# Kernel optimization log

Hardware: AMD Instinct MI355X
Metric: run time of the kernel (lower is better)

Reference implementation:

```python
import jax, jax.numpy as jnp
import numpy as np

B, ROWS, COLS, D, H = 64, 7, 7, 1280, 256
S, NEG, GRU_ROWS = 5, 16, 6  # pred_steps, neg_samples, rows processed by GRU


def setup_inputs() -> dict:
    key = jax.random.key(0)
    ks = jax.random.split(key, 10)
    sc = 0.05  # keep gates/tanh out of saturation
    return {
        "encodings": jax.random.normal(ks[0], (B, ROWS, COLS, D), jnp.float32),
        "hidden": jnp.zeros((1, 1, H), jnp.float32),
        "gru_w_ih": jax.random.normal(ks[1], (3 * H, D), jnp.float32) * sc,
        "gru_w_hh": jax.random.normal(ks[2], (3 * H, H), jnp.float32) * sc,
        "gru_b_ih": jax.random.normal(ks[3], (3 * H,), jnp.float32) * sc,
        "gru_b_hh": jax.random.normal(ks[4], (3 * H,), jnp.float32) * sc,
        "wk_w": jax.random.normal(ks[5], (S, D, H), jnp.float32) * sc,
        "wk_b": jax.random.normal(ks[6], (S, D), jnp.float32) * sc,
        "neg_rows": jax.random.randint(ks[7], (B, S, GRU_ROWS, COLS, NEG), 0, ROWS, jnp.int32),
        "neg_cols": jax.random.randint(ks[8], (B, S, GRU_ROWS, COLS, NEG), 0, COLS, jnp.int32),
    }


def _gru_contexts(encodings, hidden, w_ih, w_hh, b_ih, b_hh):
    # One GRU run per (image, column) over the first 6 rows, all batched together.
    x_seq = jnp.transpose(encodings[:, :GRU_ROWS], (1, 0, 2, 3)).reshape(GRU_ROWS, B * COLS, D)
    h0 = jnp.broadcast_to(hidden.reshape(1, H), (B * COLS, H))

    def step(h, x):
        gi = x @ w_ih.T + b_ih          # [N, 3H]
        gh = h @ w_hh.T + b_hh
        i_r, i_z, i_n = jnp.split(gi, 3, axis=-1)
        h_r, h_z, h_n = jnp.split(gh, 3, axis=-1)
        r = jax.nn.sigmoid(i_r + h_r)
        z = jax.nn.sigmoid(i_z + h_z)
        n = jnp.tanh(i_n + r * h_n)
        h_new = (1.0 - z) * n + z * h
        return h_new, h_new

    _, cs = jax.lax.scan(step, h0, x_seq)              # [6, B*7, H]
    return jnp.transpose(cs.reshape(GRU_ROWS, B, COLS, H), (1, 0, 2, 3))  # [B,6,7,H]


def reference(encodings, hidden, gru_w_ih, gru_w_hh, gru_b_ih, gru_b_hh,
              wk_w, wk_b, neg_rows, neg_cols):
    contexts = _gru_contexts(encodings, hidden, gru_w_ih, gru_w_hh, gru_b_ih, gru_b_hh)

    # Predictions for every step/row/col: hardtanh(Wk[s] c + b)   [B,S,6,7,D]
    preds = jnp.clip(jnp.einsum("brch,sdh->bsrcd", contexts, wk_w)
                     + wk_b[None, :, None, None, :], -1.0, 1.0)

    # Dot of every prediction with every patch encoding of the same image.
    enc_flat = encodings.reshape(B, ROWS * COLS, D)
    dots_all = jnp.einsum("bsrcd,bqd->bsrcq", preds, enc_flat)  # [B,S,6,7,49]

    # Positive: target is encodings[img, row, col] (as in the source).
    qpos = (jnp.arange(GRU_ROWS)[:, None] * COLS + jnp.arange(COLS)[None, :])  # [6,7]
    pos = jnp.take_along_axis(dots_all, qpos[None, None, :, :, None], axis=-1)  # [B,S,6,7,1]

    # Negatives: random (row,col) patches of the same image.
    neg_q = neg_rows * COLS + neg_cols                            # [B,S,6,7,NEG]
    neg = jnp.take_along_axis(dots_all, neg_q, axis=-1)

    dots = jnp.concatenate([pos, neg], axis=-1)                   # [B,S,6,7,1+NEG]
    loss_each = -jax.nn.log_softmax(dots, axis=-1)[..., 0]
    correct = (jnp.argmax(dots, axis=-1) == 0).astype(jnp.float32)

    # Valid predictions: row in range(6 - step)
    mask = ((jnp.arange(S)[:, None] + jnp.arange(GRU_ROWS)[None, :]) < GRU_ROWS)
    mask = mask.astype(jnp.float32)[None, :, :, None]             # [1,S,6,1]
    num_preds = jnp.sum(mask) * B * COLS

    loss = jnp.sum(loss_each * mask) / num_preds
    acc = jnp.sum(correct * mask) / num_preds
    return loss, acc
```

## Files before the change

kernel.cpp:

```cpp
#include <hip/hip_runtime.h>
#include <math.h>


typedef __bf16 bf16x8 __attribute__((ext_vector_type(8)));
typedef float  f32x4  __attribute__((ext_vector_type(4)));
typedef unsigned short u16;
typedef unsigned int u32;

__device__ inline u16 f2bf(float f) {
  unsigned int u = __float_as_uint(f);
  u += 0x7fff + ((u >> 16) & 1);
  return (u16)(u >> 16);
}

__device__ inline float bf2f(u16 b) {
  u32 u = (u32)b << 16;
  return __builtin_bit_cast(float, u);
}

__device__ inline void f2bf8(const float* s, u16* o) {
  float4 v0 = *(const float4*)s, v1 = *(const float4*)(s + 4);
  o[0] = f2bf(v0.x); o[1] = f2bf(v0.y); o[2] = f2bf(v0.z); o[3] = f2bf(v0.w);
  o[4] = f2bf(v1.x); o[5] = f2bf(v1.y); o[6] = f2bf(v1.z); o[7] = f2bf(v1.w);
}

__device__ inline bf16x8 lds_frag(const char* sm, int off) {
  return __builtin_bit_cast(bf16x8, *(const uint4*)(sm + off));
}

__device__ inline void gld_lds16(const void* g, void* l) {
  __builtin_amdgcn_global_load_lds(
      (const __attribute__((address_space(1))) u32*)g,
      (__attribute__((address_space(3))) u32*)l, 16, 0, 0);
}

__device__ inline float fast_sigmoid(float x) {
  float t = __builtin_amdgcn_exp2f(-1.44269504f * x);
  return __builtin_amdgcn_rcpf(1.f + t);
}
__device__ inline float fast_tanh(float x) {
  float xc = fminf(fmaxf(x, -9.f), 9.f);
  float t = __builtin_amdgcn_exp2f(2.88539008f * xc);
  return (t - 1.f) * __builtin_amdgcn_rcpf(t + 1.f);
}
__device__ inline float fast_exp(float x) {
  return __builtin_amdgcn_exp2f(1.44269504f * x);
}
__device__ inline float fast_log(float x) {
  return __builtin_amdgcn_logf(x) * 0.69314718f;
}

#define MFMA16(a, b, c) __builtin_amdgcn_mfma_f32_16x16x32_bf16(a, b, c, 0, 0, 0)

__global__ __launch_bounds__(256) void pack_all(
    const float* __restrict__ w_hh, const float* __restrict__ wk_w,
    const float* __restrict__ enc,  const float* __restrict__ w_ih,
    u16* __restrict__ whhpk, u16* __restrict__ wkwpk, u16* __restrict__ epk,
    u16* __restrict__ enc2,  u16* __restrict__ wih2, float* __restrict__ out)
{
  int tid = blockIdx.x * 256 + threadIdx.x;
  int lane = tid & 63;
  if (tid == 0) { out[0] = 0.f; out[1] = 0.f; }
  u16 o[8];
  if (tid < 24576) {
    int rest = tid >> 6;
    int cb = rest >> 3, ks = rest & 7;
    int w = cb / 6, nf = cb % 6;
    int g = nf >> 1, half = nf & 1;
    int col = g * 256 + w * 32 + half * 16 + (lane & 15);
    int k = ks * 32 + (lane >> 4) * 8;
    f2bf8(&w_hh[(size_t)col * 256 + k], o);
    *(uint4*)&whhpk[(size_t)tid * 8] = *(uint4*)o;
  } else if (tid < 229376) {
    int u = tid - 24576;
    int f = u >> 6;
    int ks = f & 7, t1 = f >> 3;
    int w = t1 & 3, t2 = t1 >> 2;
    int ch = t2 % 20, s = t2 / 20;
    f2bf8(&wk_w[((size_t)s * 1280 + ch * 64 + w * 16 + (lane & 15)) * 256
                + ks * 32 + (lane >> 4) * 8], o);
    *(uint4*)&wkwpk[(size_t)f * 512 + lane * 8] = *(uint4*)o;
  } else if (tid < 884736) {
    int u = tid - 229376;
    int f = u >> 6;
    int ks2 = f & 1, t1 = f >> 1;
    int w = t1 & 3, t2 = t1 >> 2;
    int ch = t2 % 20, b = t2 / 20;
    int q = w * 16 + (lane & 15);
    if (q < 49) {
      f2bf8(&enc[(size_t)(b * 49 + q) * 1280 + ch * 64 + ks2 * 32 + (lane >> 4) * 8], o);
    } else {
#pragma unroll
      for (int j = 0; j < 8; ++j) o[j] = 0;
    }
    *(uint4*)&epk[(size_t)f * 512 + lane * 8] = *(uint4*)o;
  } else if (tid < 1314816) {
    int u = tid - 884736;
    int unit = u & 1023;
    int row = unit >> 3, sl = unit & 7;
    int tk = u >> 10;
    int k0 = tk % 20, by = tk / 20;
    int m = by * 128 + row;
    int r = m / 448, n = m - r * 448;
    int b = n / 7, c = n - b * 7;
    int slot = sl ^ (row & 7);
    f2bf8(&enc[(size_t)(b * 49 + r * 7 + c) * 1280 + k0 * 64 + slot * 8], o);
    *(uint4*)&enc2[(size_t)u * 8] = *(uint4*)o;
  } else if (tid < 1437696) {
    int u = tid - 1314816;
    int unit = u & 1023;
    int row = unit >> 3, sl = unit & 7;
    int tk = u >> 10;
    int k0 = tk % 20, bx = tk / 20;
    int slot = sl ^ (row & 7);
    f2bf8(&w_ih[(size_t)(bx * 128 + row) * 1280 + k0 * 64 + slot * 8], o);
    *(uint4*)&wih2[(size_t)u * 8] = *(uint4*)o;
  }
}

__global__ __launch_bounds__(256) void gi_mfma(
    const u16* __restrict__ enc2, const u16* __restrict__ wih2,
    const float* __restrict__ b_ih, u16* __restrict__ gib)
{
  const int bx = blockIdx.x, by = blockIdx.y;
  const int t = threadIdx.x, lane = t & 63, w = t >> 6;
  const int wr = w >> 1, wc = w & 1;

  __shared__ char sm[32768];
  const int A_OFF = 0, B_OFF = 16384;
  const int wu = t & ~63;

  f32x4 acc[4][4];
#pragma unroll
  for (int i = 0; i < 4; ++i)
#pragma unroll
    for (int j = 0; j < 4; ++j) acc[i][j] = (f32x4){0.f, 0.f, 0.f, 0.f};

  for (int k0c = 0; k0c < 20; ++k0c) {
    if (k0c) __syncthreads();
    const char* ga = (const char*)enc2 + ((size_t)(by * 20 + k0c) << 14);
    const char* gb = (const char*)wih2 + ((size_t)(bx * 20 + k0c) << 14);
#pragma unroll
    for (int j = 0; j < 4; ++j) {
      gld_lds16(ga + (j * 256 + t) * 16, sm + A_OFF + (j * 256 + wu) * 16);
      gld_lds16(gb + (j * 256 + t) * 16, sm + B_OFF + (j * 256 + wu) * 16);
    }
    __syncthreads();
#pragma unroll
    for (int ks = 0; ks < 2; ++ks) {
      bf16x8 a[4], b[4];
#pragma unroll
      for (int i = 0; i < 4; ++i) {
        int arow = wr * 64 + i * 16 + (lane & 15);
        int akb  = (ks * 64 + (lane >> 4) * 16) ^ ((arow & 7) << 4);
        a[i] = lds_frag(sm, A_OFF + arow * 128 + akb);
        int brow = wc * 64 + i * 16 + (lane & 15);
        int bkb  = (ks * 64 + (lane >> 4) * 16) ^ ((brow & 7) << 4);
        b[i] = lds_frag(sm, B_OFF + brow * 128 + bkb);
      }
#pragma unroll
      for (int i = 0; i < 4; ++i)
#pragma unroll
        for (int jn = 0; jn < 4; ++jn)
          acc[i][jn] = MFMA16(a[i], b[jn], acc[i][jn]);
    }
  }

#pragma unroll
  for (int i = 0; i < 4; ++i)
#pragma unroll
    for (int jn = 0; jn < 4; ++jn) {
      int gcol = bx * 128 + wc * 64 + jn * 16 + (lane & 15);
      float bias = b_ih[gcol];
#pragma unroll
      for (int r4 = 0; r4 < 4; ++r4) {
        int grow = by * 128 + wr * 64 + i * 16 + (lane >> 4) * 4 + r4;
        gib[(size_t)grow * 768 + gcol] = f2bf(acc[i][jn][r4] + bias);
      }
    }
}

__global__ __launch_bounds__(512) void gru_fused(
    const u16* __restrict__ whh_pk, const float* __restrict__ b_hh,
    const float* __restrict__ hidden, const u16* __restrict__ gib,
    u16* __restrict__ ctxb)
{
  const int n0 = blockIdx.x * 16;
  const int t = threadIdx.x, lane = t & 63, w = t >> 6;

  __shared__ char sm[16384 + 2 * 24576];
  const int GI0 = 16384;

  const int l15 = lane & 15;
  const int seq0 = (lane >> 4) * 4;
  const int hc0 = w * 32 + l15, hc1 = w * 32 + 16 + l15;

  const float br0 = b_hh[hc0],       br1 = b_hh[hc1];
  const float bz0 = b_hh[256 + hc0], bz1 = b_hh[256 + hc1];
  const float bn0 = b_hh[512 + hc0], bn1 = b_hh[512 + hc1];

#pragma unroll
  for (int i = 0; i < 3; ++i) {
    int chunk = w * 3 + i;
    gld_lds16(gib + (size_t)n0 * 768 + chunk * 512 + lane * 8,
              sm + GI0 + chunk * 1024);
  }

  float hold[2][4];
  {
    float h0 = hidden[hc0], h1 = hidden[hc1];
#pragma unroll
    for (int r4 = 0; r4 < 4; ++r4) { hold[0][r4] = h0; hold[1][r4] = h1; }
    u16 hb0 = f2bf(h0), hb1 = f2bf(h1);
#pragma unroll
    for (int r4 = 0; r4 < 4; ++r4) {
      int seq = seq0 + r4;
      *(u16*)(sm + seq * 512 + ((hc0 * 2) ^ ((seq & 7) << 4))) = hb0;
      *(u16*)(sm + seq * 512 + ((hc1 * 2) ^ ((seq & 7) << 4))) = hb1;
    }
  }

  bf16x8 bP[3][6];
  {
    const char* pkb0 = (const char*)whh_pk + w * 49152 + lane * 16;
#pragma unroll
    for (int j = 0; j < 3; ++j)
#pragma unroll
      for (int nf = 0; nf < 6; ++nf)
        bP[j][nf] = *(const bf16x8*)(pkb0 + nf * 8192 + j * 1024);
  }
  __syncthreads();

  for (int r = 0; r < 6; ++r) {
    const char* hb  = sm + (r & 1) * 8192;
    char* hbn       = sm + ((r + 1) & 1) * 8192;
    const char* gbr = sm + GI0 + (r & 1) * 24576;

    uintptr_t pa = (uintptr_t)whh_pk;
    asm volatile("" : "+v"(pa));
    const char* pkb = (const char*)pa + w * 49152 + lane * 16;

    f32x4 acc[6];
#pragma unroll
    for (int nf = 0; nf < 6; ++nf) acc[nf] = (f32x4){0.f, 0.f, 0.f, 0.f};

#pragma unroll
    for (int ks = 0; ks < 8; ++ks) {
      const int slot = ks % 3;
      bf16x8 a = lds_frag(hb, l15 * 512 +
                          ((ks * 64 + (lane >> 4) * 16) ^ ((l15 & 7) << 4)));
#pragma unroll
      for (int nf = 0; nf < 6; ++nf) acc[nf] = MFMA16(a, bP[slot][nf], acc[nf]);
      {
        const int nk = (ks + 3) & 7;
#pragma unroll
        for (int nf = 0; nf < 6; ++nf)
          bP[slot][nf] = *(const bf16x8*)(pkb + nf * 8192 + nk * 1024);
      }
    }

    if (r + 1 < 6) {
#pragma unroll
      for (int i = 0; i < 3; ++i) {
        int chunk = w * 3 + i;
        gld_lds16(gib + (size_t)((r + 1) * 448 + n0) * 768 + chunk * 512 + lane * 8,
                  sm + GI0 + ((r + 1) & 1) * 24576 + chunk * 1024);
      }
    }

#pragma unroll
    for (int r4 = 0; r4 < 4; ++r4) {
      int seq = seq0 + r4;
      float ir0 = bf2f(*(const u16*)(gbr + (size_t)(seq * 768 + hc0) * 2));
      float iz0 = bf2f(*(const u16*)(gbr + (size_t)(seq * 768 + 256 + hc0) * 2));
      float in0 = bf2f(*(const u16*)(gbr + (size_t)(seq * 768 + 512 + hc0) * 2));
      float ir1 = bf2f(*(const u16*)(gbr + (size_t)(seq * 768 + hc1) * 2));
      float iz1 = bf2f(*(const u16*)(gbr + (size_t)(seq * 768 + 256 + hc1) * 2));
      float in1 = bf2f(*(const u16*)(gbr + (size_t)(seq * 768 + 512 + hc1) * 2));
      {
        float rg = fast_sigmoid(ir0 + acc[0][r4] + br0);
        float zg = fast_sigmoid(iz0 + acc[2][r4] + bz0);
        float ng = fast_tanh(in0 + rg * (acc[4][r4] + bn0));
        float hnew = (1.f - zg) * ng + zg * hold[0][r4];
        hold[0][r4] = hnew;
        u16 hb16 = f2bf(hnew);
        *(u16*)(hbn + seq * 512 + ((hc0 * 2) ^ ((seq & 7) << 4))) = hb16;
        ctxb[(size_t)(r * 448 + n0 + seq) * 256 + hc0] = hb16;
      }
      {
        float rg = fast_sigmoid(ir1 + acc[1][r4] + br1);
        float zg = fast_sigmoid(iz1 + acc[3][r4] + bz1);
        float ng = fast_tanh(in1 + rg * (acc[5][r4] + bn1));
        float hnew = (1.f - zg) * ng + zg * hold[1][r4];
        hold[1][r4] = hnew;
        u16 hb16 = f2bf(hnew);
        *(u16*)(hbn + seq * 512 + ((hc1 * 2) ^ ((seq & 7) << 4))) = hb16;
        ctxb[(size_t)(r * 448 + n0 + seq) * 256 + hc1] = hb16;
      }
    }
    __syncthreads();
  }
}

template<int MF>
__device__ __forceinline__ void pd_body(
    int b, int s, int Ms, int t, int lane, int w, char* sm,
    const u16* __restrict__ ctxb, const u16* __restrict__ wkwpk,
    const float* __restrict__ wk_b, const u16* __restrict__ epk,
    const int* __restrict__ neg_rows, const int* __restrict__ neg_cols,
    float* __restrict__ out)
{
  const int PT_OFF = 24576;

#pragma unroll
  for (int j = 0; j < 6; ++j) {
    int u = j * 256 + t;
    int row = u >> 5, slot = u & 31;
    int rr = row < Ms ? row : 0;
    int r = rr / 7, c = rr - r * 7;
    uint4 v = *(const uint4*)&ctxb[((size_t)(r * 448 + b * 7 + c)) * 256 + slot * 8];
    int off = row * 512 + ((slot * 16) ^ ((row & 7) << 4));
    *(uint4*)(sm + off) = v;
  }
  __syncthreads();

  bf16x8 a1[MF][8];
#pragma unroll
  for (int m = 0; m < MF; ++m)
#pragma unroll
    for (int ks = 0; ks < 8; ++ks) {
      int row = m * 16 + (lane & 15);
      int kb  = (ks * 64 + (lane >> 4) * 16) ^ ((row & 7) << 4);
      a1[m][ks] = lds_frag(sm, row * 512 + kb);
    }

  f32x4 acc2[MF];
#pragma unroll
  for (int m = 0; m < MF; ++m) acc2[m] = (f32x4){0.f, 0.f, 0.f, 0.f};

  const char* wfB = (const char*)wkwpk + ((size_t)(s * 20) * 4 + w) * 8192 + lane * 16;
  const char* efB = (const char*)epk   + ((size_t)(b * 20) * 4 + w) * 2048 + lane * 16;
  const int colL = w * 16 + (lane & 15);

  bf16x8 wF[8];
#pragma unroll
  for (int ks = 0; ks < 8; ++ks)
    wF[ks] = *(const bf16x8*)(wfB + ks * 1024);

  for (int ch = 0; ch < 20; ++ch) {
    char* pt = sm + PT_OFF + (ch & 1) * 6144;

    f32x4 acc1[MF];
#pragma unroll
    for (int m = 0; m < MF; ++m) acc1[m] = (f32x4){0.f, 0.f, 0.f, 0.f};
#pragma unroll
    for (int ks = 0; ks < 8; ++ks) {
#pragma unroll
      for (int m = 0; m < MF; ++m) acc1[m] = MFMA16(a1[m][ks], wF[ks], acc1[m]);
    }
    if (ch + 1 < 20) {
      const char* wfn = wfB + (size_t)(ch + 1) * 4 * 8192;
#pragma unroll
      for (int ks = 0; ks < 8; ++ks)
        wF[ks] = *(const bf16x8*)(wfn + ks * 1024);
    }
    {
      float bias = wk_b[s * 1280 + ch * 64 + colL];
#pragma unroll
      for (int m = 0; m < MF; ++m)
#pragma unroll
        for (int r4 = 0; r4 < 4; ++r4) {
          float p = acc1[m][r4] + bias;
          p = fminf(fmaxf(p, -1.f), 1.f);
          int prow = m * 16 + (lane >> 4) * 4 + r4;
          *(u16*)(pt + prow * 128 + ((colL * 2) ^ ((prow & 7) << 4))) = f2bf(p);
        }
    }
    const char* ef = efB + (size_t)ch * 4 * 2048;
    bf16x8 e0 = *(const bf16x8*)ef;
    bf16x8 e1 = *(const bf16x8*)(ef + 1024);
    __syncthreads();

#pragma unroll
    for (int m = 0; m < MF; ++m) {
      int prow = m * 16 + (lane & 15);
      bf16x8 pf0 = lds_frag(pt, prow * 128 +
                            (((lane >> 4) * 16) ^ ((prow & 7) << 4)));
      acc2[m] = MFMA16(pf0, e0, acc2[m]);
      bf16x8 pf1 = lds_frag(pt, prow * 128 +
                            ((64 + (lane >> 4) * 16) ^ ((prow & 7) << 4)));
      acc2[m] = MFMA16(pf1, e1, acc2[m]);
    }
  }

  float* dtile = (float*)sm;
#pragma unroll
  for (int m = 0; m < MF; ++m)
#pragma unroll
    for (int r4 = 0; r4 < 4; ++r4) {
      int row = m * 16 + (lane >> 4) * 4 + r4;
      int q = w * 16 + (lane & 15);
      dtile[row * 65 + q] = acc2[m][r4];
    }
  __syncthreads();

  if (w == 0) {
    float lsum = 0.f, csum = 0.f;
    if (lane < Ms) {
      int rr = lane;
      int r = rr / 7, c = rr - r * 7;
      const float* drow = &dtile[rr * 65];
      float d0 = drow[rr];
      const int nbase = (((b * 5 + s) * 6 + r) * 7 + c) * 16;
      float mx = d0;
      float d[16];
#pragma unroll
      for (int j = 0; j < 16; ++j) {
        int q = neg_rows[nbase + j] * 7 + neg_cols[nbase + j];
        d[j] = drow[q];
        mx = fmaxf(mx, d[j]);
      }
      float se = fast_exp(d0 - mx);
#pragma unroll
      for (int j = 0; j < 16; ++j) se += fast_exp(d[j] - mx);
      lsum = -(d0 - mx - fast_log(se));
      csum = (d0 >= mx) ? 1.f : 0.f;
    }
#pragma unroll
    for (int off = 32; off > 0; off >>= 1) {
      lsum += __shfl_down(lsum, off);
      csum += __shfl_down(csum, off);
    }
    if (lane == 0) {
      atomicAdd(&out[0], lsum * (1.f / 8960.f));
      atomicAdd(&out[1], csum * (1.f / 8960.f));
    }
  }
}

__global__ __launch_bounds__(256) void fused_pd(
    const u16* __restrict__ ctxb, const u16* __restrict__ wkwpk,
    const float* __restrict__ wk_b, const u16* __restrict__ epk,
    const int* __restrict__ neg_rows, const int* __restrict__ neg_cols,
    float* __restrict__ out)
{
  const int b = blockIdx.x;
  const int s = blockIdx.y;
  const int Ms = (6 - s) * 7;
  const int t = threadIdx.x;
  const int lane = t & 63, w = t >> 6;

  __shared__ uint4 smem4[36864 / 16];
  char* sm = (char*)smem4;

  if (s < 2)      pd_body<3>(b, s, Ms, t, lane, w, sm, ctxb, wkwpk, wk_b, epk,
                             neg_rows, neg_cols, out);
  else if (s < 4) pd_body<2>(b, s, Ms, t, lane, w, sm, ctxb, wkwpk, wk_b, epk,
                             neg_rows, neg_cols, out);
  else            pd_body<1>(b, s, Ms, t, lane, w, sm, ctxb, wkwpk, wk_b, epk,
                             neg_rows, neg_cols, out);
}

extern "C" void kernel_launch(void* const* d_in, const int* in_sizes, int n_in,
                              void* d_out, int out_size, void* d_ws, size_t ws_size,
                              hipStream_t stream)
{
  const float* enc    = (const float*)d_in[0];
  const float* hidden = (const float*)d_in[1];
  const float* w_ih   = (const float*)d_in[2];
  const float* w_hh   = (const float*)d_in[3];
  const float* b_ih   = (const float*)d_in[4];
  const float* b_hh   = (const float*)d_in[5];
  const float* wk_w   = (const float*)d_in[6];
  const float* wk_b   = (const float*)d_in[7];
  const int* neg_rows = (const int*)d_in[8];
  const int* neg_cols = (const int*)d_in[9];
  float* out = (float*)d_out;

  u16*   gib   = (u16*)d_ws;
  u16*   ctxb  = gib + 6 * 448 * 768;
  u16*   whhpk = ctxb + 6 * 448 * 256;
  u16*   wkwpk = whhpk + 24576 * 8;
  u16*   epk   = wkwpk + 204800 * 8;
  u16*   enc2  = epk + 655360 * 8;
  u16*   wih2  = enc2 + 430080 * 8;

  pack_all<<<5616, 256, 0, stream>>>(w_hh, wk_w, enc, w_ih,
                                     whhpk, wkwpk, epk, enc2, wih2, out);

  gi_mfma<<<dim3(6, 21), 256, 0, stream>>>(enc2, wih2, b_ih, gib);

  gru_fused<<<28, 512, 0, stream>>>(whhpk, b_hh, hidden, gib, ctxb);

  fused_pd<<<dim3(64, 5), 256, 0, stream>>>(ctxb, wkwpk, wk_b, epk,
                                            neg_rows, neg_cols, out);
}
```

Before: 98.18 us.

## Merge encoding packing passes and double-buffer LDS loads in gi_mfma

pack_all now reads each encoding chunk once and writes both the epk layout and the swizzled enc2 layout from the same converted registers. This removes a second full read and conversion of the encodings and shrinks the grid. Separately, gi_mfma now uses two LDS buffers, prefetching the next K-chunk with global-to-LDS loads while computing on the current one, with an explicit vmcnt wait and raw barriers. This doubles LDS use to 64KB per block, which may lower occupancy.

After: 92.12 us. 1.07x faster.

```diff
diff --git a/kernel.cpp b/kernel.cpp
--- a/kernel.cpp
+++ b/kernel.cpp
@@ -62,17 +62,40 @@
   int lane = tid & 63;
   if (tid == 0) { out[0] = 0.f; out[1] = 0.f; }
   u16 o[8];
-  if (tid < 24576) {
-    int rest = tid >> 6;
+  if (tid < 655360) {
+    int f = tid >> 6;
+    int ks2 = f & 1, t1 = f >> 1;
+    int w = t1 & 3, t2 = t1 >> 2;
+    int ch = t2 % 20, b = t2 / 20;
+    int q = w * 16 + (lane & 15);
+    int d = ch * 64 + ks2 * 32 + (lane >> 4) * 8;
+    if (q < 49) {
+      f2bf8(&enc[(size_t)(b * 49 + q) * 1280 + d], o);
+    } else {
+#pragma unroll
+      for (int j = 0; j < 8; ++j) o[j] = 0;
+    }
+    *(uint4*)&epk[(size_t)f * 512 + lane * 8] = *(uint4*)o;
+    if (q < 42) {
+      int r = q / 7, c = q - r * 7;
+      int m = r * 448 + b * 7 + c;
+      int by = m >> 7, row = m & 127;
+      int k0 = d >> 6, slot = (d & 63) >> 3;
+      int sl = slot ^ (row & 7);
+      *(uint4*)&enc2[(size_t)((by * 20 + k0) * 1024 + row * 8 + sl) * 8] = *(uint4*)o;
+    }
+  } else if (tid < 679936) {
+    int u = tid - 655360;
+    int rest = u >> 6;
     int cb = rest >> 3, ks = rest & 7;
     int w = cb / 6, nf = cb % 6;
     int g = nf >> 1, half = nf & 1;
     int col = g * 256 + w * 32 + half * 16 + (lane & 15);
     int k = ks * 32 + (lane >> 4) * 8;
     f2bf8(&w_hh[(size_t)col * 256 + k], o);
-    *(uint4*)&whhpk[(size_t)tid * 8] = *(uint4*)o;
-  } else if (tid < 229376) {
-    int u = tid - 24576;
+    *(uint4*)&whhpk[(size_t)u * 8] = *(uint4*)o;
+  } else if (tid < 884736) {
+    int u = tid - 679936;
     int f = u >> 6;
     int ks = f & 7, t1 = f >> 3;
     int w = t1 & 3, t2 = t1 >> 2;
@@ -80,34 +103,8 @@
     f2bf8(&wk_w[((size_t)s * 1280 + ch * 64 + w * 16 + (lane & 15)) * 256
                 + ks * 32 + (lane >> 4) * 8], o);
     *(uint4*)&wkwpk[(size_t)f * 512 + lane * 8] = *(uint4*)o;
-  } else if (tid < 884736) {
-    int u = tid - 229376;
-    int f = u >> 6;
-    int ks2 = f & 1, t1 = f >> 1;
-    int w = t1 & 3, t2 = t1 >> 2;
-    int ch = t2 % 20, b = t2 / 20;
-    int q = w * 16 + (lane & 15);
-    if (q < 49) {
-      f2bf8(&enc[(size_t)(b * 49 + q) * 1280 + ch * 64 + ks2 * 32 + (lane >> 4) * 8], o);
-    } else {
-#pragma unroll
-      for (int j = 0; j < 8; ++j) o[j] = 0;
-    }
-    *(uint4*)&epk[(size_t)f * 512 + lane * 8] = *(uint4*)o;
-  } else if (tid < 1314816) {
+  } else if (tid < 1007616) {
     int u = tid - 884736;
-    int unit = u & 1023;
-    int row = unit >> 3, sl = unit & 7;
-    int tk = u >> 10;
-    int k0 = tk % 20, by = tk / 20;
-    int m = by * 128 + row;
-    int r = m / 448, n = m - r * 448;
-    int b = n / 7, c = n - b * 7;
-    int slot = sl ^ (row & 7);
-    f2bf8(&enc[(size_t)(b * 49 + r * 7 + c) * 1280 + k0 * 64 + slot * 8], o);
-    *(uint4*)&enc2[(size_t)u * 8] = *(uint4*)o;
-  } else if (tid < 1437696) {
-    int u = tid - 1314816;
     int unit = u & 1023;
     int row = unit >> 3, sl = unit & 7;
     int tk = u >> 10;
@@ -126,8 +123,7 @@
   const int t = threadIdx.x, lane = t & 63, w = t >> 6;
   const int wr = w >> 1, wc = w & 1;
 
-  __shared__ char sm[32768];
-  const int A_OFF = 0, B_OFF = 16384;
+  __shared__ char sm[65536];
   const int wu = t & ~63;
 
   f32x4 acc[4][4];
@@ -136,16 +132,32 @@
 #pragma unroll
     for (int j = 0; j < 4; ++j) acc[i][j] = (f32x4){0.f, 0.f, 0.f, 0.f};
 
+  const char* ga0 = (const char*)enc2 + ((size_t)(by * 20) << 14);
+  const char* gb0 = (const char*)wih2 + ((size_t)(bx * 20) << 14);
+
+#pragma unroll
+  for (int j = 0; j < 4; ++j) {
+    gld_lds16(ga0 + (j * 256 + t) * 16, sm + (j * 256 + wu) * 16);
+    gld_lds16(gb0 + (j * 256 + t) * 16, sm + 16384 + (j * 256 + wu) * 16);
+  }
+
   for (int k0c = 0; k0c < 20; ++k0c) {
-    if (k0c) __syncthreads();
-    const char* ga = (const char*)enc2 + ((size_t)(by * 20 + k0c) << 14);
-    const char* gb = (const char*)wih2 + ((size_t)(bx * 20 + k0c) << 14);
-#pragma unroll
-    for (int j = 0; j < 4; ++j) {
-      gld_lds16(ga + (j * 256 + t) * 16, sm + A_OFF + (j * 256 + wu) * 16);
-      gld_lds16(gb + (j * 256 + t) * 16, sm + B_OFF + (j * 256 + wu) * 16);
-    }
-    __syncthreads();
+    char* cur = sm + (k0c & 1) * 32768;
+    if (k0c + 1 < 20) {
+      char* nxt = sm + ((k0c + 1) & 1) * 32768;
+      const char* ga = ga0 + ((size_t)(k0c + 1) << 14);
+      const char* gb = gb0 + ((size_t)(k0c + 1) << 14);
+#pragma unroll
+      for (int j = 0; j < 4; ++j) {
+        gld_lds16(ga + (j * 256 + t) * 16, nxt + (j * 256 + wu) * 16);
+        gld_lds16(gb + (j * 256 + t) * 16, nxt + 16384 + (j * 256 + wu) * 16);
+      }
+      asm volatile("s_waitcnt vmcnt(8)" ::: "memory");
+    } else {
+      asm volatile("s_waitcnt vmcnt(0)" ::: "memory");
+    }
+    __builtin_amdgcn_s_barrier();
+
 #pragma unroll
     for (int ks = 0; ks < 2; ++ks) {
       bf16x8 a[4], b[4];
@@ -153,10 +165,10 @@
       for (int i = 0; i < 4; ++i) {
         int arow = wr * 64 + i * 16 + (lane & 15);
         int akb  = (ks * 64 + (lane >> 4) * 16) ^ ((arow & 7) << 4);
-        a[i] = lds_frag(sm, A_OFF + arow * 128 + akb);
+        a[i] = lds_frag(cur, arow * 128 + akb);
         int brow = wc * 64 + i * 16 + (lane & 15);
         int bkb  = (ks * 64 + (lane >> 4) * 16) ^ ((brow & 7) << 4);
-        b[i] = lds_frag(sm, B_OFF + brow * 128 + bkb);
+        b[i] = lds_frag(cur + 16384, brow * 128 + bkb);
       }
 #pragma unroll
       for (int i = 0; i < 4; ++i)
@@ -164,6 +176,7 @@
         for (int jn = 0; jn < 4; ++jn)
           acc[i][jn] = MFMA16(a[i], b[jn], acc[i][jn]);
     }
+    __builtin_amdgcn_s_barrier();
   }
 
 #pragma unroll
@@ -485,7 +498,7 @@
   u16*   enc2  = epk + 655360 * 8;
   u16*   wih2  = enc2 + 430080 * 8;
 
-  pack_all<<<5616, 256, 0, stream>>>(w_hh, wk_w, enc, w_ih,
+  pack_all<<<3936, 256, 0, stream>>>(w_hh, wk_w, enc, w_ih,
                                      whhpk, wkwpk, epk, enc2, wih2, out);
 
   gi_mfma<<<dim3(6, 21), 256, 0, stream>>>(enc2, wih2, b_ih, gib);
```
